# Kernel tuning notes

Measured on AMD Instinct MI355X. Metric: run time of the kernel, lower is better.

The kernel has to match this reference:

```python
import jax, jax.numpy as jnp
import numpy as np

B, T, L = 4096, 512, 16


def setup_inputs() -> dict:
    key = jax.random.key(0)
    k1, k2, k3, k4 = jax.random.split(key, 4)
    x = jax.random.normal(k1, (B, T, L), dtype=jnp.float32)
    trans = jax.random.uniform(k2, (L, L), dtype=jnp.float32)
    label = jax.random.randint(k3, (B, T), 0, L, dtype=jnp.int32)
    length = jax.random.randint(k4, (B,), 1, T + 1, dtype=jnp.int32)
    return {"x": x, "trans": trans, "label": label, "length": length}


def _crf_loss(x, trans, label, length):
    b, t, l = x.shape
    # valid-position mask [B, T]
    mask = (jnp.arange(t)[None, :] < length[:, None]).astype(x.dtype)
    x = x * mask[:, :, None]  # mask emissions like the original

    # ---- gold path score ----
    # emission (point) score: sum_t x[b, t, label[b, t]] over valid t
    emit = jnp.take_along_axis(x, label[:, :, None].astype(jnp.int32), axis=2)[..., 0]
    point_score = jnp.sum(emit * mask, axis=1, keepdims=True)  # [B, 1]
    # transition score: sum over consecutive valid label pairs
    pair_mask = mask[:, 1:]  # both t and t+1 valid iff t+1 valid (monotone mask)
    trans_pairs = trans[label[:, :-1], label[:, 1:]]  # [B, T-1]
    trans_score = jnp.sum(trans_pairs * pair_mask, axis=1, keepdims=True)  # [B, 1]
    label_score = point_score + trans_score  # [B, 1]

    # ---- partition function via forward algorithm (scan over time) ----
    alpha0 = x[:, 0, :]  # [B, L]
    xs = jnp.swapaxes(x[:, 1:, :], 0, 1)  # [T-1, B, L]

    def step(alpha, x_t):
        # logsumexp over previous label axis of alpha[b, i] + trans[i, j]
        new = jax.nn.logsumexp(alpha[:, :, None] + trans[None, :, :], axis=1) + x_t
        return new, new

    _, ys = jax.lax.scan(step, alpha0, xs)  # ys: [T-1, B, L]
    alphas = jnp.concatenate([alpha0[None], ys], axis=0)  # [T, B, L]
    # pick alpha at t = length - 1 for each batch element
    final = alphas[length - 1, jnp.arange(b), :]  # [B, L]
    z = jax.nn.logsumexp(final, axis=1, keepdims=True)  # [B, 1]
    return z - label_score


def reference(x, trans, label, length):
    return _crf_loss(x, trans, label, length)
```

## Files before the change

kernel.cpp:

```cpp
#include <hip/hip_runtime.h>
#include <cstdint>


static constexpr float L2E = 1.4426950408889634f;
static constexpr float LN2 = 0.69314718055994531f;

__device__ __forceinline__ void gload_lds16(const void* g, void* l) {
  __builtin_amdgcn_global_load_lds((const __attribute__((address_space(1))) unsigned int*)g,
                                   (__attribute__((address_space(3))) unsigned int*)l, 16, 0, 0);
}
__device__ __forceinline__ void gload_lds4(const void* g, void* l) {
  __builtin_amdgcn_global_load_lds((const __attribute__((address_space(1))) unsigned int*)g,
                                   (__attribute__((address_space(3))) unsigned int*)l, 4, 0, 0);
}
__device__ __forceinline__ void wait_vm0() { asm volatile("s_waitcnt vmcnt(0)" ::: "memory"); }
__device__ __forceinline__ void wait_vm5() { asm volatile("s_waitcnt vmcnt(5)" ::: "memory"); }

template <int CTRL>
__device__ __forceinline__ float dppf(float v) {
  return __builtin_bit_cast(float,
      __builtin_amdgcn_mov_dpp(__builtin_bit_cast(int, v), CTRL, 0xF, 0xF, true));
}
template <int CTRL>
__device__ __forceinline__ int dppi(int v) {
  return __builtin_amdgcn_mov_dpp(v, CTRL, 0xF, 0xF, true);
}
__device__ __forceinline__ float rfl(float v) {
  return __builtin_bit_cast(float, __builtin_amdgcn_readfirstlane(__builtin_bit_cast(int, v)));
}

__global__ __launch_bounds__(256, 4) void crf_fwd(
    const float* __restrict__ x, const float* __restrict__ trans,
    const int* __restrict__ label, const int* __restrict__ length,
    float* __restrict__ out) {
  __shared__ float ldsx[4][2][64 * 16];
  __shared__ int   ldsl[4][2][64];
  __shared__ float ldst[256];

  const int tid  = threadIdx.x;
  const int wv   = tid >> 6;
  const int lane = tid & 63;
  const int l16  = lane & 15;

  ldst[tid] = trans[tid];
  __syncthreads();

  const int b   = blockIdx.x * 4 + wv;
  const int len = length[b];
  const int nch = ((len - 1) >> 6) + 1;

  const int i1  = dppi<0x121>(l16);
  const int i2  = dppi<0x122>(l16);
  const int i3  = dppi<0x123>(l16);
  const int i4  = dppi<0x124>(l16);
  const int i5  = dppi<0x125>(l16);
  const int i6  = dppi<0x126>(l16);
  const int i7  = dppi<0x127>(l16);
  const int i8  = dppi<0x128>(l16);
  const int i9  = dppi<0x129>(l16);
  const int i10 = dppi<0x12A>(l16);
  const int i11 = dppi<0x12B>(l16);
  const int i12 = dppi<0x12C>(l16);
  const int i13 = dppi<0x12D>(l16);
  const int i14 = dppi<0x12E>(l16);
  const int i15 = dppi<0x12F>(l16);
  const float m0  = __builtin_amdgcn_exp2f(trans[l16 * 16 + l16] * L2E);
  const float m1  = __builtin_amdgcn_exp2f(trans[i1  * 16 + l16] * L2E);
  const float m2  = __builtin_amdgcn_exp2f(trans[i2  * 16 + l16] * L2E);
  const float m3  = __builtin_amdgcn_exp2f(trans[i3  * 16 + l16] * L2E);
  const float m4  = __builtin_amdgcn_exp2f(trans[i4  * 16 + l16] * L2E);
  const float m5  = __builtin_amdgcn_exp2f(trans[i5  * 16 + l16] * L2E);
  const float m6  = __builtin_amdgcn_exp2f(trans[i6  * 16 + l16] * L2E);
  const float m7  = __builtin_amdgcn_exp2f(trans[i7  * 16 + l16] * L2E);
  const float m8  = __builtin_amdgcn_exp2f(trans[i8  * 16 + l16] * L2E);
  const float m9  = __builtin_amdgcn_exp2f(trans[i9  * 16 + l16] * L2E);
  const float m10 = __builtin_amdgcn_exp2f(trans[i10 * 16 + l16] * L2E);
  const float m11 = __builtin_amdgcn_exp2f(trans[i11 * 16 + l16] * L2E);
  const float m12 = __builtin_amdgcn_exp2f(trans[i12 * 16 + l16] * L2E);
  const float m13 = __builtin_amdgcn_exp2f(trans[i13 * 16 + l16] * L2E);
  const float m14 = __builtin_amdgcn_exp2f(trans[i14 * 16 + l16] * L2E);
  const float m15 = __builtin_amdgcn_exp2f(trans[i15 * 16 + l16] * L2E);

  const char* xb = (const char*)x + (size_t)b * 32768;
  const char* lb = (const char*)label + (size_t)b * 2048;

  auto stage = [&](int c, int buf) {
    const char* gx = xb + c * 4096;
    float* lxp = &ldsx[wv][buf][0];
    gload_lds16(gx + 0 * 1024 + lane * 16, lxp + 0 * 256);
    gload_lds16(gx + 1 * 1024 + lane * 16, lxp + 1 * 256);
    gload_lds16(gx + 2 * 1024 + lane * 16, lxp + 2 * 256);
    gload_lds16(gx + 3 * 1024 + lane * 16, lxp + 3 * 256);
    gload_lds4(lb + c * 256 + lane * 4, &ldsl[wv][buf][0]);
  };

  stage(0, 0);

  float av = 1.0f;
  float R2 = 0.0f;
  float em = 0.0f;
  float ts = 0.0f;
  int lastl = 0;

  auto step = [&](float xe) {
    float a0 = av * m0;
    float a1 = dppf<0x124>(av) * m4;
    float a2 = dppf<0x128>(av) * m8;
    float a3 = dppf<0x12C>(av) * m12;
    a0 = __builtin_fmaf(dppf<0x121>(av), m1,  a0);
    a1 = __builtin_fmaf(dppf<0x125>(av), m5,  a1);
    a2 = __builtin_fmaf(dppf<0x129>(av), m9,  a2);
    a3 = __builtin_fmaf(dppf<0x12D>(av), m13, a3);
    a0 = __builtin_fmaf(dppf<0x122>(av), m2,  a0);
    a1 = __builtin_fmaf(dppf<0x126>(av), m6,  a1);
    a2 = __builtin_fmaf(dppf<0x12A>(av), m10, a2);
    a3 = __builtin_fmaf(dppf<0x12E>(av), m14, a3);
    a0 = __builtin_fmaf(dppf<0x123>(av), m3,  a0);
    a1 = __builtin_fmaf(dppf<0x127>(av), m7,  a1);
    a2 = __builtin_fmaf(dppf<0x12B>(av), m11, a2);
    a3 = __builtin_fmaf(dppf<0x12F>(av), m15, a3);
    av = ((a0 + a1) + (a2 + a3)) * xe;
  };
  auto renorm = [&]() {
    const float C = rfl(av);
    av *= __builtin_amdgcn_rcpf(C);
    R2 += __builtin_amdgcn_logf(C);
  };

  for (int c = 0; c < nch; ++c) {
    const int buf = c & 1;
    const bool pre = (c + 1 < nch);
    if (pre) stage(c + 1, buf ^ 1);
    if (pre) wait_vm5(); else wait_vm0();

    float* lx = &ldsx[wv][buf][0];
    int*   ll = &ldsl[wv][buf][0];

    {
      const int gt   = c * 64 + lane;
      const int lblt = ll[lane];
      const int lprv = (lane == 0) ? lastl : ll[lane - 1];
      const float emv = lx[lane * 16 + lblt];
      const float tsv = ldst[lprv * 16 + lblt];
      if (gt < len) em += emv;
      if (gt >= 1 && gt < len) ts += tsv;
      lastl = __shfl(lblt, 63, 64);
    }

    {
      float4* p = (float4*)(lx + lane * 16);
#pragma unroll
      for (int k = 0; k < 4; ++k) {
        float4 v = p[k];
        v.x = __builtin_amdgcn_exp2f(v.x * L2E);
        v.y = __builtin_amdgcn_exp2f(v.y * L2E);
        v.z = __builtin_amdgcn_exp2f(v.z * L2E);
        v.w = __builtin_amdgcn_exp2f(v.w * L2E);
        p[k] = v;
      }
    }

    if (c == 0) av = lx[l16];

    const int start = (c == 0) ? 1 : c * 64;
    const int end   = (len - 1 < c * 64 + 63) ? (len - 1) : (c * 64 + 63);
    int n = end - start + 1;
    if (n > 0) {
      const float* xp = lx + (start & 63) * 16 + l16;
      while (n >= 4) {
        step(xp[0]);
        step(xp[16]);
        step(xp[32]);
        step(xp[48]);
        xp += 64;
        n -= 4;
        renorm();
      }
      if (n > 0) {
        for (int e = 0; e < n; ++e) step(xp[e * 16]);
        renorm();
      }
    }
  }

  float stot = av;
  stot += dppf<0x128>(stot);
  stot += dppf<0x124>(stot);
  stot += dppf<0x122>(stot);
  stot += dppf<0x121>(stot);

  em += __shfl_xor(em, 1, 64);
  em += __shfl_xor(em, 2, 64);
  em += __shfl_xor(em, 4, 64);
  em += __shfl_xor(em, 8, 64);
  em += __shfl_xor(em, 16, 64);
  em += __shfl_xor(em, 32, 64);

  ts += __shfl_xor(ts, 1, 64);
  ts += __shfl_xor(ts, 2, 64);
  ts += __shfl_xor(ts, 4, 64);
  ts += __shfl_xor(ts, 8, 64);
  ts += __shfl_xor(ts, 16, 64);
  ts += __shfl_xor(ts, 32, 64);

  const float z2 = R2 + __builtin_amdgcn_logf(stot);
  const float res = z2 * LN2 - em - ts;
  if (lane == 0) out[b] = res;
}

extern "C" void kernel_launch(void* const* d_in, const int* in_sizes, int n_in,
                              void* d_out, int out_size, void* d_ws, size_t ws_size,
                              hipStream_t stream) {
  const float* x      = (const float*)d_in[0];
  const float* trans  = (const float*)d_in[1];
  const int*   label  = (const int*)d_in[2];
  const int*   length = (const int*)d_in[3];
  float* out = (float*)d_out;
  const int B = in_sizes[3];
  crf_fwd<<<dim3(B / 4), dim3(256), 0, stream>>>(x, trans, label, length, out);
}
```

Before: 269.5 us.

## Pack four batch rows per wavefront and use exponent-only renormalization

Each wavefront now handles four batch elements, one per 16-lane row, instead of one element with 48 idle lanes in the recurrence. The chain runs to the max length of the four rows, masking updates past each row's length. Renormalization now sums the row with DPP and rescales by a power of two taken from the exponent bits, which avoids log and rcp. Per-wave LDS staging quadruples, so the launch bound drops to one block, which lowers occupancy and can waste steps when lengths differ within a group.

```diff
diff --git a/kernel.cpp b/kernel.cpp
--- a/kernel.cpp
+++ b/kernel.cpp
@@ -13,8 +13,6 @@
   __builtin_amdgcn_global_load_lds((const __attribute__((address_space(1))) unsigned int*)g,
                                    (__attribute__((address_space(3))) unsigned int*)l, 4, 0, 0);
 }
-__device__ __forceinline__ void wait_vm0() { asm volatile("s_waitcnt vmcnt(0)" ::: "memory"); }
-__device__ __forceinline__ void wait_vm5() { asm volatile("s_waitcnt vmcnt(5)" ::: "memory"); }
 
 template <int CTRL>
 __device__ __forceinline__ float dppf(float v) {
@@ -25,29 +23,32 @@
 __device__ __forceinline__ int dppi(int v) {
   return __builtin_amdgcn_mov_dpp(v, CTRL, 0xF, 0xF, true);
 }
-__device__ __forceinline__ float rfl(float v) {
-  return __builtin_bit_cast(float, __builtin_amdgcn_readfirstlane(__builtin_bit_cast(int, v)));
-}
-
-__global__ __launch_bounds__(256, 4) void crf_fwd(
+
+__global__ __launch_bounds__(256, 1) void crf_fwd(
     const float* __restrict__ x, const float* __restrict__ trans,
     const int* __restrict__ label, const int* __restrict__ length,
     float* __restrict__ out) {
-  __shared__ float ldsx[4][2][64 * 16];
-  __shared__ int   ldsl[4][2][64];
+  __shared__ float ldsx[4][2][4 * 1032];
+  __shared__ int   ldsl[4][2][4][64];
   __shared__ float ldst[256];
 
   const int tid  = threadIdx.x;
   const int wv   = tid >> 6;
   const int lane = tid & 63;
   const int l16  = lane & 15;
+  const int row  = lane >> 4;
 
   ldst[tid] = trans[tid];
   __syncthreads();
 
-  const int b   = blockIdx.x * 4 + wv;
-  const int len = length[b];
-  const int nch = ((len - 1) >> 6) + 1;
+  const int wb0   = blockIdx.x * 16 + wv * 4;
+  const int myb   = wb0 + row;
+  const int mylen = length[myb];
+  int mx = mylen;
+  { int o = __shfl_xor(mx, 16, 64); mx = mx > o ? mx : o; }
+  { int o = __shfl_xor(mx, 32, 64); mx = mx > o ? mx : o; }
+  const int maxlen = __builtin_amdgcn_readfirstlane(mx);
+  const int nch = ((maxlen - 1) >> 6) + 1;
 
   const int i1  = dppi<0x121>(l16);
   const int i2  = dppi<0x122>(l16);
@@ -81,105 +82,122 @@
   const float m14 = __builtin_amdgcn_exp2f(trans[i14 * 16 + l16] * L2E);
   const float m15 = __builtin_amdgcn_exp2f(trans[i15 * 16 + l16] * L2E);
 
-  const char* xb = (const char*)x + (size_t)b * 32768;
-  const char* lb = (const char*)label + (size_t)b * 2048;
-
   auto stage = [&](int c, int buf) {
-    const char* gx = xb + c * 4096;
-    float* lxp = &ldsx[wv][buf][0];
-    gload_lds16(gx + 0 * 1024 + lane * 16, lxp + 0 * 256);
-    gload_lds16(gx + 1 * 1024 + lane * 16, lxp + 1 * 256);
-    gload_lds16(gx + 2 * 1024 + lane * 16, lxp + 2 * 256);
-    gload_lds16(gx + 3 * 1024 + lane * 16, lxp + 3 * 256);
-    gload_lds4(lb + c * 256 + lane * 4, &ldsl[wv][buf][0]);
+#pragma unroll
+    for (int q = 0; q < 4; ++q) {
+      const char* gx = (const char*)x + (size_t)(wb0 + q) * 32768 + (size_t)c * 4096;
+      float* dst = &ldsx[wv][buf][q * 1032];
+      gload_lds16(gx + 0 * 1024 + lane * 16, dst + 0 * 256);
+      gload_lds16(gx + 1 * 1024 + lane * 16, dst + 1 * 256);
+      gload_lds16(gx + 2 * 1024 + lane * 16, dst + 2 * 256);
+      gload_lds16(gx + 3 * 1024 + lane * 16, dst + 3 * 256);
+      gload_lds4((const char*)label + (size_t)(wb0 + q) * 2048 + (size_t)c * 256 + lane * 4,
+                 &ldsl[wv][buf][q][0]);
+    }
   };
 
   stage(0, 0);
 
   float av = 1.0f;
-  float R2 = 0.0f;
-  float em = 0.0f;
-  float ts = 0.0f;
+  int   R2 = 0;
+  float em = 0.0f, ts = 0.0f;
   int lastl = 0;
-
-  auto step = [&](float xe) {
-    float a0 = av * m0;
-    float a1 = dppf<0x124>(av) * m4;
-    float a2 = dppf<0x128>(av) * m8;
-    float a3 = dppf<0x12C>(av) * m12;
-    a0 = __builtin_fmaf(dppf<0x121>(av), m1,  a0);
-    a1 = __builtin_fmaf(dppf<0x125>(av), m5,  a1);
-    a2 = __builtin_fmaf(dppf<0x129>(av), m9,  a2);
-    a3 = __builtin_fmaf(dppf<0x12D>(av), m13, a3);
-    a0 = __builtin_fmaf(dppf<0x122>(av), m2,  a0);
-    a1 = __builtin_fmaf(dppf<0x126>(av), m6,  a1);
-    a2 = __builtin_fmaf(dppf<0x12A>(av), m10, a2);
-    a3 = __builtin_fmaf(dppf<0x12E>(av), m14, a3);
-    a0 = __builtin_fmaf(dppf<0x123>(av), m3,  a0);
-    a1 = __builtin_fmaf(dppf<0x127>(av), m7,  a1);
-    a2 = __builtin_fmaf(dppf<0x12B>(av), m11, a2);
-    a3 = __builtin_fmaf(dppf<0x12F>(av), m15, a3);
-    av = ((a0 + a1) + (a2 + a3)) * xe;
-  };
+  int t = 1;
+
   auto renorm = [&]() {
-    const float C = rfl(av);
-    av *= __builtin_amdgcn_rcpf(C);
-    R2 += __builtin_amdgcn_logf(C);
+    float C = av;
+    C += dppf<0x128>(C);
+    C += dppf<0x124>(C);
+    C += dppf<0x122>(C);
+    C += dppf<0x121>(C);
+    const int biased = (__builtin_bit_cast(int, C) >> 23) & 0xFF;
+    av *= __builtin_bit_cast(float, (254 - biased) << 23);
+    R2 += biased - 127;
   };
 
   for (int c = 0; c < nch; ++c) {
     const int buf = c & 1;
-    const bool pre = (c + 1 < nch);
-    if (pre) stage(c + 1, buf ^ 1);
-    if (pre) wait_vm5(); else wait_vm0();
-
-    float* lx = &ldsx[wv][buf][0];
-    int*   ll = &ldsl[wv][buf][0];
+    if (c + 1 < nch) {
+      stage(c + 1, buf ^ 1);
+      asm volatile("s_waitcnt vmcnt(20)" ::: "memory");
+    } else {
+      asm volatile("s_waitcnt vmcnt(0)" ::: "memory");
+    }
+
+    float* xreg = &ldsx[wv][buf][row * 1032];
+    int*   ll   = &ldsl[wv][buf][row][0];
 
     {
-      const int gt   = c * 64 + lane;
-      const int lblt = ll[lane];
-      const int lprv = (lane == 0) ? lastl : ll[lane - 1];
-      const float emv = lx[lane * 16 + lblt];
-      const float tsv = ldst[lprv * 16 + lblt];
-      if (gt < len) em += emv;
-      if (gt >= 1 && gt < len) ts += tsv;
-      lastl = __shfl(lblt, 63, 64);
-    }
-
-    {
-      float4* p = (float4*)(lx + lane * 16);
-#pragma unroll
-      for (int k = 0; k < 4; ++k) {
-        float4 v = p[k];
+      const int t0 = 4 * l16;
+      const int4 lb4 = *(const int4*)&ll[t0];
+      int prev = (l16 == 0) ? lastl : ll[t0 - 1];
+      const int gt0 = c * 64 + t0;
+      const int lbls[4] = {lb4.x, lb4.y, lb4.z, lb4.w};
+#pragma unroll
+      for (int u = 0; u < 4; ++u) {
+        const int gt  = gt0 + u;
+        const int lbl = lbls[u];
+        if (gt < mylen) {
+          em += xreg[(t0 + u) * 16 + lbl];
+          if (gt >= 1) ts += ldst[prev * 16 + lbl];
+        }
+        prev = lbl;
+      }
+      lastl = __shfl(lb4.w, (lane & 48) + 15, 64);
+    }
+
+#pragma unroll
+    for (int q = 0; q < 4; ++q) {
+      float4* p = (float4*)&ldsx[wv][buf][q * 1032];
+#pragma unroll
+      for (int f = 0; f < 4; ++f) {
+        float4 v = p[f * 64 + lane];
         v.x = __builtin_amdgcn_exp2f(v.x * L2E);
         v.y = __builtin_amdgcn_exp2f(v.y * L2E);
         v.z = __builtin_amdgcn_exp2f(v.z * L2E);
         v.w = __builtin_amdgcn_exp2f(v.w * L2E);
-        p[k] = v;
+        p[f * 64 + lane] = v;
       }
     }
 
-    if (c == 0) av = lx[l16];
-
-    const int start = (c == 0) ? 1 : c * 64;
-    const int end   = (len - 1 < c * 64 + 63) ? (len - 1) : (c * 64 + 63);
-    int n = end - start + 1;
-    if (n > 0) {
-      const float* xp = lx + (start & 63) * 16 + l16;
-      while (n >= 4) {
-        step(xp[0]);
-        step(xp[16]);
-        step(xp[32]);
-        step(xp[48]);
-        xp += 64;
-        n -= 4;
-        renorm();
-      }
-      if (n > 0) {
-        for (int e = 0; e < n; ++e) step(xp[e * 16]);
-        renorm();
-      }
+    if (c == 0) av = xreg[l16];
+
+    int tend = c * 64 + 63;
+    if (tend > maxlen - 1) tend = maxlen - 1;
+    const float* xp = &xreg[(t & 63) * 16 + l16];
+
+    auto stepf = [&]() {
+      const float xe = *xp;
+      xp += 16;
+      float a0 = av * m0;
+      float a1 = dppf<0x124>(av) * m4;
+      float a2 = dppf<0x128>(av) * m8;
+      float a3 = dppf<0x12C>(av) * m12;
+      a0 = __builtin_fmaf(dppf<0x121>(av), m1,  a0);
+      a1 = __builtin_fmaf(dppf<0x125>(av), m5,  a1);
+      a2 = __builtin_fmaf(dppf<0x129>(av), m9,  a2);
+      a3 = __builtin_fmaf(dppf<0x12D>(av), m13, a3);
+      a0 = __builtin_fmaf(dppf<0x122>(av), m2,  a0);
+      a1 = __builtin_fmaf(dppf<0x126>(av), m6,  a1);
+      a2 = __builtin_fmaf(dppf<0x12A>(av), m10, a2);
+      a3 = __builtin_fmaf(dppf<0x12E>(av), m14, a3);
+      a0 = __builtin_fmaf(dppf<0x123>(av), m3,  a0);
+      a1 = __builtin_fmaf(dppf<0x127>(av), m7,  a1);
+      a2 = __builtin_fmaf(dppf<0x12B>(av), m11, a2);
+      a3 = __builtin_fmaf(dppf<0x12F>(av), m15, a3);
+      const float acc = ((a0 + a1) + (a2 + a3)) * xe;
+      av = (t < mylen) ? acc : av;
+      ++t;
+    };
+
+    while (t + 7 <= tend) {
+#pragma unroll
+      for (int u = 0; u < 8; ++u) stepf();
+      renorm();
+    }
+    if (t <= tend) {
+      while (t <= tend) stepf();
+      renorm();
     }
   }
 
@@ -193,19 +211,14 @@
   em += __shfl_xor(em, 2, 64);
   em += __shfl_xor(em, 4, 64);
   em += __shfl_xor(em, 8, 64);
-  em += __shfl_xor(em, 16, 64);
-  em += __shfl_xor(em, 32, 64);
-
   ts += __shfl_xor(ts, 1, 64);
   ts += __shfl_xor(ts, 2, 64);
   ts += __shfl_xor(ts, 4, 64);
   ts += __shfl_xor(ts, 8, 64);
-  ts += __shfl_xor(ts, 16, 64);
-  ts += __shfl_xor(ts, 32, 64);
-
-  const float z2 = R2 + __builtin_amdgcn_logf(stot);
+
+  const float z2  = (float)R2 + __builtin_amdgcn_logf(stot);
   const float res = z2 * LN2 - em - ts;
-  if (lane == 0) out[b] = res;
+  if (l16 == 0) out[myb] = res;
 }
 
 extern "C" void kernel_launch(void* const* d_in, const int* in_sizes, int n_in,
@@ -217,5 +230,5 @@
   const int*   length = (const int*)d_in[3];
   float* out = (float*)d_out;
   const int B = in_sizes[3];
-  crf_fwd<<<dim3(B / 4), dim3(256), 0, stream>>>(x, trans, label, length, out);
-}
+  crf_fwd<<<dim3(B / 16), dim3(256), 0, stream>>>(x, trans, label, length, out);
+}
```

Result: faster. 228.9 us (-15.1%).
